# Kernel tuning notes

Hardware: AMD Instinct MI355X
Metric: run time of the kernel (lower is better)

## Reference

```python
import jax, jax.numpy as jnp
import numpy as np

N_NODES = 100000
IN_F = 128
H_F = 128
LOOKBACK = 3
N_EDGES = 640000


def setup_inputs() -> dict:
    key = jax.random.key(0)
    ks = jax.random.split(key, 16)
    s = lambda k, shp: jax.random.normal(k, shp, dtype=jnp.float32) * 0.05
    inp = {
        "feat": jax.random.normal(ks[0], (N_NODES, IN_F), dtype=jnp.float32),
        "edges": jax.random.randint(ks[1], (LOOKBACK, 2, N_EDGES), 0, N_NODES, dtype=jnp.int32),
        # conv1 (SAGEConv pool, in->h) params
        "Wp1": s(ks[2], (IN_F, IN_F)), "bp1": jnp.zeros((IN_F,), jnp.float32),
        "Ws1": s(ks[3], (H_F, IN_F)), "Wn1": s(ks[4], (H_F, IN_F)), "b1": jnp.zeros((H_F,), jnp.float32),
        # BatchNorm1d affine params (training-mode batch stats)
        "gamma": jnp.ones((H_F,), jnp.float32), "beta": jnp.zeros((H_F,), jnp.float32),
        # conv2 (SAGEConv pool, h->h) params
        "Wp2": s(ks[5], (H_F, H_F)), "bp2": jnp.zeros((H_F,), jnp.float32),
        "Ws2": s(ks[6], (H_F, H_F)), "Wn2": s(ks[7], (H_F, H_F)), "b2": jnp.zeros((H_F,), jnp.float32),
    }
    return inp


def _sage_pool_conv(h, src, dst, Wp, bp, Ws, Wn, b):
    # pool aggregator: m = relu(fc_pool(h)); neigh = max over in-edges
    m = jax.nn.relu(h @ Wp.T + bp)                      # [N, d]
    agg = jax.ops.segment_max(m[src], dst, num_segments=N_NODES)  # [N, d]
    agg = jnp.where(jnp.isfinite(agg), agg, 0.0)        # nodes with no in-edges -> 0
    return h @ Ws.T + agg @ Wn.T + b


def _batchnorm(x, gamma, beta, eps=1e-5):
    mu = jnp.mean(x, axis=0)
    var = jnp.var(x, axis=0)
    return (x - mu) * jax.lax.rsqrt(var + eps) * gamma + beta


def reference(feat, edges, Wp1, bp1, Ws1, Wn1, b1, gamma, beta, Wp2, bp2, Ws2, Wn2, b2):
    def per_graph(e):
        src, dst = e[0], e[1]
        h = _sage_pool_conv(feat, src, dst, Wp1, bp1, Ws1, Wn1, b1)
        h = _batchnorm(h, gamma, beta)
        h = jax.nn.relu(h)
        h = _sage_pool_conv(h, src, dst, Wp2, bp2, Ws2, Wn2, b2)
        return h

    return jax.vmap(per_graph)(edges)  # [lookback, N, H_F]
```

## Files before the change

### kernel.cpp

```cpp
#include <hip/hip_runtime.h>
#include <hip/hip_bf16.h>

#define NNODES 100000
#define FD 128
#define NEDGES 640000
#define NB 391
#define NT64 1563
#define GX_TWOA 85
#define GX_ONEW 170
#define GX_HEAD 255
#define OFFS_U32 100032

typedef __bf16 bf16x8 __attribute__((ext_vector_type(8)));
typedef __bf16 bf16x4 __attribute__((ext_vector_type(4)));
typedef float f32x4 __attribute__((ext_vector_type(4)));
typedef unsigned short u16x8 __attribute__((ext_vector_type(8)));

__device__ __forceinline__ bf16x8 cvt8(float4 a, float4 b) {
  bf16x8 r;
  r[0] = (__bf16)a.x; r[1] = (__bf16)a.y; r[2] = (__bf16)a.z; r[3] = (__bf16)a.w;
  r[4] = (__bf16)b.x; r[5] = (__bf16)b.y; r[6] = (__bf16)b.z; r[7] = (__bf16)b.w;
  return r;
}

__device__ __forceinline__ void gl16(const void* g, void* l) {
  __builtin_amdgcn_global_load_lds(
      (const __attribute__((address_space(1))) unsigned int*)g,
      (__attribute__((address_space(3))) unsigned int*)l, 16, 0, 0);
}

__device__ __forceinline__ void stage_w32(const __bf16* Wp, char* l, int wid, int lane) {
#pragma unroll
  for (int i = 0; i < 4; ++i) {
    const int off = (wid * 4 + i) * 1024;
    gl16((const char*)Wp + off + lane * 16, l + off);
  }
}

__device__ __forceinline__ void stage_abf(const __bf16* A, long row0, int M,
                                          char* l, int wid, int lane) {
  long row = row0 + lane;
  if (row > M - 1) row = M - 1;
  const char* base = (const char*)(A + row * FD);
#pragma unroll
  for (int i = 0; i < 2; ++i) {
    const int s = wid * 2 + i;
    gl16(base + s * 16, l + s * 1024);
  }
}

__device__ __forceinline__ void stage_a32(const float* A, long row0, int M,
                                          char* l, int wid, int lane) {
  long row = row0 + lane;
  if (row > M - 1) row = M - 1;
  const char* base = (const char*)(A + row * FD);
#pragma unroll
  for (int i = 0; i < 4; ++i) {
    const int s = wid * 4 + i;
    gl16(base + s * 16, l + s * 1024);
  }
}

__global__ __launch_bounds__(256) void packw6_k(
    const float* __restrict__ W0, const float* __restrict__ W1,
    const float* __restrict__ W2, const float* __restrict__ W3,
    const float* __restrict__ W4, const float* __restrict__ W5,
    __bf16* __restrict__ out) {
  const int gidx = blockIdx.x * 256 + threadIdx.x;
  const int wi = gidx >> 11;
  const int f = gidx & 2047;
  const float* W = wi == 0 ? W0 : wi == 1 ? W1 : wi == 2 ? W2
                 : wi == 3 ? W3 : wi == 4 ? W4 : W5;
  const int c = f >> 8, kk = (f >> 6) & 3, lane = f & 63;
  const int lr = lane & 15, lg = lane >> 4;
  const float* p = W + (c * 16 + lr) * FD + kk * 32 + lg * 8;
  *(bf16x8*)(out + (long)gidx * 8) = cvt8(*(const float4*)p, *(const float4*)(p + 4));
}

template <int AM>
__device__ __forceinline__ void lds_arow(const char* l, int rl, int lg,
                                         const float* __restrict__ scsh,
                                         bf16x8 (&af)[4]) {
#pragma unroll
  for (int kk = 0; kk < 4; ++kk) {
    if constexpr (AM == 0) {
      const int s = kk * 8 + lg * 2;
      const float4 x = *(const float4*)(l + s * 1024 + rl * 16);
      const float4 y = *(const float4*)(l + (s + 1) * 1024 + rl * 16);
      af[kk] = cvt8(x, y);
    } else {
      const bf16x8 r = *(const bf16x8*)(l + (kk * 4 + lg) * 1024 + rl * 16);
      if constexpr (AM == 3) {
        const int k = lg * 8 + kk * 32;
        const float4 scx = *(const float4*)(scsh + k);
        const float4 scy = *(const float4*)(scsh + k + 4);
        const float4 shx = *(const float4*)(scsh + 128 + k);
        const float4 shy = *(const float4*)(scsh + 128 + k + 4);
        bf16x8 o;
        o[0] = (__bf16)fmaxf((float)r[0] * scx.x + shx.x, 0.f);
        o[1] = (__bf16)fmaxf((float)r[1] * scx.y + shx.y, 0.f);
        o[2] = (__bf16)fmaxf((float)r[2] * scx.z + shx.z, 0.f);
        o[3] = (__bf16)fmaxf((float)r[3] * scx.w + shx.w, 0.f);
        o[4] = (__bf16)fmaxf((float)r[4] * scy.x + shy.x, 0.f);
        o[5] = (__bf16)fmaxf((float)r[5] * scy.y + shy.y, 0.f);
        o[6] = (__bf16)fmaxf((float)r[6] * scy.z + shy.z, 0.f);
        o[7] = (__bf16)fmaxf((float)r[7] * scy.w + shy.w, 0.f);
        af[kk] = o;
      } else {
        af[kk] = r;
      }
    }
  }
}

template <int A0M, int A1M, bool TWOA, bool RELU, bool OUTBF16, bool STATS, bool WRITEB>
__global__ __launch_bounds__(512, 1) void gemm_k(
    const void* __restrict__ A0, long a0s, const void* __restrict__ A1, long a1s,
    const __bf16* __restrict__ W0p, const __bf16* __restrict__ W1p,
    const float* __restrict__ bias, const float* __restrict__ scsh0,
    void* __restrict__ outp, long os, float* __restrict__ pblk,
    __bf16* __restrict__ bcopy, int M) {
  constexpr int WSZ = TWOA ? 65536 : 32768;
  constexpr int ASZ = (A0M == 0) ? 32768 : 16384;
  constexpr int A1SZ = TWOA ? 16384 : 0;
  constexpr int LSZ = WSZ + 2 * (ASZ + A1SZ) + (STATS ? 4096 : 0);
  __shared__ __align__(16) char lds[LSZ];
  char* lW0 = lds;
  char* lW1 = lds + 32768;
  char* lA0a = lds + WSZ;
  char* lA1a = lds + WSZ + ASZ;
  char* lA0b = lds + WSZ + ASZ + A1SZ;
  char* lA1b = lds + WSZ + ASZ + A1SZ + ASZ;
  float* s_red = (float*)(lds + WSZ + 2 * (ASZ + A1SZ));

  const int g = blockIdx.y;
  const int tid = threadIdx.x;
  const int wid = tid >> 6;
  const int lane = tid & 63;
  const int rw = wid & 3;
  const int cw = wid >> 2;
  const int lr = lane & 15;
  const int lg = lane >> 4;
  const int S = gridDim.x;

  const void* A0g = (const char*)A0 + (long)g * a0s;
  const void* A1g = (const char*)A1 + (TWOA ? (long)g * a1s : 0);
  void* outg = (char*)outp + (long)g * os;
  const float* scshg = (A0M == 3 || A1M == 3) ? scsh0 + (long)g * 256 : nullptr;

  float ps[4][4], pss[4][4];
  if constexpr (STATS) {
#pragma unroll
    for (int ci = 0; ci < 4; ++ci)
#pragma unroll
      for (int j = 0; j < 4; ++j) { ps[ci][j] = 0.f; pss[ci][j] = 0.f; }
  }

  auto stageA = [&](long t, char* la0, char* la1) {
    if constexpr (A0M == 0) stage_a32((const float*)A0g, t * 64, M, la0, wid, lane);
    else stage_abf((const __bf16*)A0g, t * 64, M, la0, wid, lane);
    if constexpr (TWOA) stage_abf((const __bf16*)A1g, t * 64, M, la1, wid, lane);
  };

  auto body = [&](long t, long tn, char* la0, char* la1, char* na0, char* na1) {
    if (tn < NT64) stageA(tn, na0, na1);
    const int rl = rw * 16 + lr;
    const long row = t * 64 + rl;
    const bool ok = row < M;

    bf16x8 a0f[4];
    lds_arow<A0M>(la0, rl, lg, scshg, a0f);
    bf16x8 a1f[4];
    if constexpr (TWOA) lds_arow<A1M>(la1, rl, lg, scshg, a1f);

    if constexpr (WRITEB) {
      if (cw == 0 && ok) {
#pragma unroll
        for (int kk = 0; kk < 4; ++kk)
          *(bf16x8*)(bcopy + row * FD + lg * 8 + kk * 32) = a0f[kk];
      }
    }

    f32x4 acc[4];
#pragma unroll
    for (int ci = 0; ci < 4; ++ci) acc[ci] = (f32x4){0.f, 0.f, 0.f, 0.f};

#pragma unroll
    for (int ci = 0; ci < 4; ++ci) {
      bf16x8 bw[4];
#pragma unroll
      for (int kk = 0; kk < 4; ++kk)
        bw[kk] = *(const bf16x8*)(lW0 + ((cw * 4 + ci) * 4 + kk) * 1024 + lane * 16);
#pragma unroll
      for (int kk = 0; kk < 4; ++kk)
        acc[ci] = __builtin_amdgcn_mfma_f32_16x16x32_bf16(bw[kk], a0f[kk], acc[ci], 0, 0, 0);
    }
    if constexpr (TWOA) {
#pragma unroll
      for (int ci = 0; ci < 4; ++ci) {
        bf16x8 bw[4];
#pragma unroll
        for (int kk = 0; kk < 4; ++kk)
          bw[kk] = *(const bf16x8*)(lW1 + ((cw * 4 + ci) * 4 + kk) * 1024 + lane * 16);
#pragma unroll
        for (int kk = 0; kk < 4; ++kk)
          acc[ci] = __builtin_amdgcn_mfma_f32_16x16x32_bf16(bw[kk], a1f[kk], acc[ci], 0, 0, 0);
      }
    }

#pragma unroll
    for (int ci = 0; ci < 4; ++ci) {
      const int cb = cw * 64 + ci * 16 + lg * 4;
      f32x4 v = acc[ci];
      if (bias) {
        const float4 bv = *(const float4*)(bias + cb);
        v[0] += bv.x; v[1] += bv.y; v[2] += bv.z; v[3] += bv.w;
      }
      if constexpr (STATS) {
        if (ok) {
#pragma unroll
          for (int j = 0; j < 4; ++j) { ps[ci][j] += v[j]; pss[ci][j] += v[j] * v[j]; }
        }
      }
      if constexpr (RELU) {
#pragma unroll
        for (int j = 0; j < 4; ++j) v[j] = fmaxf(v[j], 0.f);
      }
      if (ok) {
        if constexpr (OUTBF16) {
          bf16x4 o;
          o[0] = (__bf16)v[0]; o[1] = (__bf16)v[1];
          o[2] = (__bf16)v[2]; o[3] = (__bf16)v[3];
          *(bf16x4*)((__bf16*)outg + row * FD + cb) = o;
        } else {
          *(f32x4*)((float*)outg + row * FD + cb) = v;
        }
      }
    }
    __syncthreads();
  };

  stage_w32(W0p, lW0, wid, lane);
  if constexpr (TWOA) stage_w32(W1p, lW1, wid, lane);
  long t = blockIdx.x;
  stageA(t, lA0a, lA1a);
  __syncthreads();

  for (;;) {
    long tn = t + S;
    body(t, tn, lA0a, lA1a, lA0b, lA1b);
    t = tn;
    if (t >= NT64) break;
    tn = t + S;
    body(t, tn, lA0b, lA1b, lA0a, lA1a);
    t = tn;
    if (t >= NT64) break;
  }

  if constexpr (STATS) {
#pragma unroll
    for (int ci = 0; ci < 4; ++ci)
#pragma unroll
      for (int j = 0; j < 4; ++j) {
        float s = ps[ci][j], q = pss[ci][j];
        s += __shfl_xor(s, 1); s += __shfl_xor(s, 2);
        s += __shfl_xor(s, 4); s += __shfl_xor(s, 8);
        q += __shfl_xor(q, 1); q += __shfl_xor(q, 2);
        q += __shfl_xor(q, 4); q += __shfl_xor(q, 8);
        if (lr == 0) {
          s_red[(0 * 8 + wid) * 64 + ci * 16 + lg * 4 + j] = s;
          s_red[(1 * 8 + wid) * 64 + ci * 16 + lg * 4 + j] = q;
        }
      }
    __syncthreads();
    if (tid < 256) {
      const int which = tid >> 7, col = tid & 127;
      const int cwi = col >> 6, cl = col & 63;
      float a = 0.f;
#pragma unroll
      for (int r = 0; r < 4; ++r) a += s_red[(which * 8 + cwi * 4 + r) * 64 + cl];
      pblk[((long)g * gridDim.x + blockIdx.x) * 256 + tid] = a;
    }
  }
}

__global__ __launch_bounds__(256) void bn_final2_k(const float* __restrict__ pblk,
                                                   const float* __restrict__ gamma,
                                                   const float* __restrict__ beta,
                                                   float* __restrict__ scsh3) {
  __shared__ float s_ss[128];
  const int g = blockIdx.y;
  const int tid = threadIdx.x;
  const float* p = pblk + (long)g * GX_TWOA * 256;
  float s = 0.f;
  for (int r = 0; r < GX_TWOA; ++r) s += p[r * 256 + tid];
  if (tid >= 128) s_ss[tid - 128] = s;
  __syncthreads();
  if (tid < 128) {
    const float mu = s / (float)NNODES;
    const float var = s_ss[tid] / (float)NNODES - mu * mu;
    const float sc = rsqrtf(var + 1e-5f) * gamma[tid];
    scsh3[g * 256 + tid] = sc;
    scsh3[g * 256 + 128 + tid] = beta[tid] - mu * sc;
  }
}


__global__ __launch_bounds__(256) void hist_rank3_k(const int* __restrict__ edges,
                                                    unsigned* __restrict__ deg3,
                                                    unsigned short* __restrict__ rank3) {
  const int g = blockIdx.y;
  const int e = blockIdx.x * 256 + threadIdx.x;
  if (e < NEDGES) {
    const int d = edges[(long)g * 2 * NEDGES + NEDGES + e];
    const unsigned r = atomicAdd(&deg3[(long)g * NNODES + d], 1u);
    rank3[(long)g * NEDGES + e] = (unsigned short)r;
  }
}

__global__ __launch_bounds__(256) void blocksum3_k(const unsigned* __restrict__ deg3,
                                                   unsigned* __restrict__ bsum3) {
  __shared__ unsigned s[256];
  const int g = blockIdx.y;
  const int i = blockIdx.x * 256 + threadIdx.x;
  s[threadIdx.x] = (i < NNODES) ? deg3[(long)g * NNODES + i] : 0u;
  __syncthreads();
#pragma unroll
  for (int o = 128; o > 0; o >>= 1) {
    if (threadIdx.x < o) s[threadIdx.x] += s[threadIdx.x + o];
    __syncthreads();
  }
  if (threadIdx.x == 0) bsum3[g * NB + blockIdx.x] = s[0];
}

__global__ __launch_bounds__(512) void scanb3_k(const unsigned* __restrict__ bsum3,
                                                unsigned* __restrict__ boffs3,
                                                unsigned* __restrict__ offs3) {
  __shared__ unsigned s[512];
  const int g = blockIdx.y;
  const unsigned v = (threadIdx.x < NB) ? bsum3[g * NB + threadIdx.x] : 0u;
  s[threadIdx.x] = v;
  __syncthreads();
#pragma unroll
  for (int o = 1; o < 512; o <<= 1) {
    unsigned t = (threadIdx.x >= o) ? s[threadIdx.x - o] : 0u;
    __syncthreads();
    s[threadIdx.x] += t;
    __syncthreads();
  }
  if (threadIdx.x < NB) boffs3[g * NB + threadIdx.x] = s[threadIdx.x] - v;
  if (threadIdx.x == 0) offs3[(long)g * OFFS_U32 + NNODES] = NEDGES;
}

__global__ __launch_bounds__(256) void offsets3_k(const unsigned* __restrict__ deg3,
                                                  const unsigned* __restrict__ boffs3,
                                                  unsigned* __restrict__ offs3) {
  __shared__ unsigned s[256];
  const int g = blockIdx.y;
  const int i = blockIdx.x * 256 + threadIdx.x;
  const unsigned v = (i < NNODES) ? deg3[(long)g * NNODES + i] : 0u;
  s[threadIdx.x] = v;
  __syncthreads();
#pragma unroll
  for (int o = 1; o < 256; o <<= 1) {
    unsigned t = (threadIdx.x >= o) ? s[threadIdx.x - o] : 0u;
    __syncthreads();
    s[threadIdx.x] += t;
    __syncthreads();
  }
  const unsigned excl = s[threadIdx.x] - v + boffs3[g * NB + blockIdx.x];
  if (i < NNODES) offs3[(long)g * OFFS_U32 + i] = excl;
}

__global__ __launch_bounds__(256) void scat3_k(const int* __restrict__ edges,
                                               const unsigned* __restrict__ offs3,
                                               const unsigned short* __restrict__ rank3,
                                               int* __restrict__ ssrc3) {
  const int g = blockIdx.y;
  const int e = blockIdx.x * 256 + threadIdx.x;
  if (e < NEDGES) {
    const int s = edges[(long)g * 2 * NEDGES + e];
    const int d = edges[(long)g * 2 * NEDGES + NEDGES + e];
    const unsigned p = offs3[(long)g * OFFS_U32 + d] + rank3[(long)g * NEDGES + e];
    ssrc3[(long)g * NEDGES + p] = s;
  }
}

__global__ __launch_bounds__(256) void agg_k(const unsigned short* __restrict__ m,
                                             long ms, const int* __restrict__ ssrc3,
                                             const unsigned* __restrict__ offs3,
                                             unsigned short* __restrict__ agg3) {
  const int g = blockIdx.y;
  const unsigned short* mg = m + (long)g * ms;
  const int* ssrc = ssrc3 + (long)g * NEDGES;
  const unsigned* offs = offs3 + (long)g * OFFS_U32;
  unsigned short* agg = agg3 + (long)g * NNODES * FD;

  const int gid = blockIdx.x * 256 + threadIdx.x;
  const int node = gid >> 4;
  if (node >= NNODES) return;
  const int fl = (gid & 15) * 8;
  const unsigned beg = offs[node], end = offs[node + 1];
  u16x8 acc = {0, 0, 0, 0, 0, 0, 0, 0};
  unsigned i = beg;
  for (; i + 2 <= end; i += 2) {
    const int s0 = ssrc[i];
    const int s1 = ssrc[i + 1];
    const u16x8 v0 = *(const u16x8*)(mg + (long)s0 * FD + fl);
    const u16x8 v1 = *(const u16x8*)(mg + (long)s1 * FD + fl);
#pragma unroll
    for (int j = 0; j < 8; ++j) {
      const unsigned short mx = v0[j] > v1[j] ? v0[j] : v1[j];
      acc[j] = mx > acc[j] ? mx : acc[j];
    }
  }
  if (i < end) {
    const u16x8 v = *(const u16x8*)(mg + (long)ssrc[i] * FD + fl);
#pragma unroll
    for (int j = 0; j < 8; ++j) acc[j] = v[j] > acc[j] ? v[j] : acc[j];
  }
  *(u16x8*)(agg + (long)node * FD + fl) = acc;
}

__global__ __launch_bounds__(256) void zero_k(float4* __restrict__ p, long n4) {
  const long i = (long)blockIdx.x * 256 + threadIdx.x;
  if (i < n4) p[i] = (float4){0.f, 0.f, 0.f, 0.f};
}

extern "C" void kernel_launch(void* const* d_in, const int* in_sizes, int n_in,
                              void* d_out, int out_size, void* d_ws, size_t ws_size,
                              hipStream_t stream) {
  const float* feat = (const float*)d_in[0];
  const int* edges = (const int*)d_in[1];
  const float* Wp1 = (const float*)d_in[2];
  const float* bp1 = (const float*)d_in[3];
  const float* Ws1 = (const float*)d_in[4];
  const float* Wn1 = (const float*)d_in[5];
  const float* b1 = (const float*)d_in[6];
  const float* gamma = (const float*)d_in[7];
  const float* beta = (const float*)d_in[8];
  const float* Wp2 = (const float*)d_in[9];
  const float* bp2 = (const float*)d_in[10];
  const float* Ws2 = (const float*)d_in[11];
  const float* Wn2 = (const float*)d_in[12];
  const float* b2 = (const float*)d_in[13];

  const long SZ_BF = 25600000;
  const long SZ_F32 = 51200000;

  char* w = (char*)d_ws;
  __bf16* m1 = (__bf16*)w;
  __bf16* featb = (__bf16*)(w + 25600000);
  __bf16* h1b3 = (__bf16*)(w + 51200000);
  __bf16* aggb3 = (__bf16*)(w + 128000000);
  __bf16* m2_3 = (__bf16*)(w + 204800000);
  float* pblk3 = (float*)(w + 204800000);
  __bf16* wpk = (__bf16*)(w + 281600000);
  float* scsh3 = (float*)(w + 281796608);
  unsigned* deg3 = (unsigned*)(w + 281799680);
  unsigned* offs3 = (unsigned*)(w + 282999680);
  unsigned* bsum3 = (unsigned*)(w + 284200064);
  unsigned* boffs3 = (unsigned*)(w + 284204928);
  unsigned short* rank3 = (unsigned short*)(w + 284209792);
  int* ssrc3 = (int*)(w + 288049792);

  __bf16* Wp1p = wpk;
  __bf16* Ws1p = wpk + 16384;
  __bf16* Wn1p = wpk + 2 * 16384;
  __bf16* Wp2p = wpk + 3 * 16384;
  __bf16* Ws2p = wpk + 4 * 16384;
  __bf16* Wn2p = wpk + 5 * 16384;

  const dim3 blk(256);
  const dim3 blk512(512);
  const int edgeGrid = (NEDGES + 255) / 256;
  const int aggGrid = (NNODES * 16 + 255) / 256;
  const int degZeroGrid = (3 * NNODES / 4 + 255) / 256;

  packw6_k<<<48, blk, 0, stream>>>(Wp1, Ws1, Wn1, Wp2, Ws2, Wn2, wpk);

  zero_k<<<degZeroGrid, blk, 0, stream>>>((float4*)deg3, 3L * NNODES / 4);
  hist_rank3_k<<<dim3(edgeGrid, 3), blk, 0, stream>>>(edges, deg3, rank3);
  blocksum3_k<<<dim3(NB, 3), blk, 0, stream>>>(deg3, bsum3);
  scanb3_k<<<dim3(1, 3), dim3(512), 0, stream>>>(bsum3, boffs3, offs3);
  offsets3_k<<<dim3(NB, 3), blk, 0, stream>>>(deg3, boffs3, offs3);
  scat3_k<<<dim3(edgeGrid, 3), blk, 0, stream>>>(edges, offs3, rank3, ssrc3);

  gemm_k<0, 0, false, true, true, false, true><<<dim3(GX_HEAD, 1), blk512, 0, stream>>>(
      feat, 0, nullptr, 0, Wp1p, nullptr, bp1, nullptr, m1, 0, nullptr, featb, NNODES);

  agg_k<<<dim3(aggGrid, 3), blk, 0, stream>>>((const unsigned short*)m1, 0L,
                                              ssrc3, offs3, (unsigned short*)aggb3);
  gemm_k<1, 1, true, false, true, true, false><<<dim3(GX_TWOA, 3), blk512, 0, stream>>>(
      aggb3, SZ_BF, featb, 0, Wn1p, Ws1p, b1, nullptr, h1b3, SZ_BF, pblk3, nullptr, NNODES);
  bn_final2_k<<<dim3(1, 3), blk, 0, stream>>>(pblk3, gamma, beta, scsh3);

  gemm_k<3, 0, false, true, true, false, false><<<dim3(GX_ONEW, 3), blk512, 0, stream>>>(
      h1b3, SZ_BF, nullptr, 0, Wp2p, nullptr, bp2, scsh3, m2_3, SZ_BF, nullptr, nullptr, NNODES);
  agg_k<<<dim3(aggGrid, 3), blk, 0, stream>>>((const unsigned short*)m2_3,
                                              (long)NNODES * FD, ssrc3, offs3,
                                              (unsigned short*)aggb3);
  gemm_k<3, 1, true, false, false, false, false><<<dim3(GX_TWOA, 3), blk512, 0, stream>>>(
      h1b3, SZ_BF, aggb3, SZ_BF, Ws2p, Wn2p, b2, scsh3, d_out, SZ_F32, nullptr, nullptr, NNODES);
}
```

Baseline: 519.0 us.

## Hold GEMM weights in registers, drop LDS weight staging, double occupancy

```diff
diff --git a/kernel.cpp b/kernel.cpp
--- a/kernel.cpp
+++ b/kernel.cpp
@@ -6,9 +6,9 @@
 #define NEDGES 640000
 #define NB 391
 #define NT64 1563
-#define GX_TWOA 85
-#define GX_ONEW 170
-#define GX_HEAD 255
+#define GX_TWOA 170
+#define GX_ONEW 340
+#define GX_HEAD 512
 #define OFFS_U32 100032
 
 typedef __bf16 bf16x8 __attribute__((ext_vector_type(8)));
@@ -27,14 +27,6 @@
   __builtin_amdgcn_global_load_lds(
       (const __attribute__((address_space(1))) unsigned int*)g,
       (__attribute__((address_space(3))) unsigned int*)l, 16, 0, 0);
-}
-
-__device__ __forceinline__ void stage_w32(const __bf16* Wp, char* l, int wid, int lane) {
-#pragma unroll
-  for (int i = 0; i < 4; ++i) {
-    const int off = (wid * 4 + i) * 1024;
-    gl16((const char*)Wp + off + lane * 16, l + off);
-  }
 }
 
 __device__ __forceinline__ void stage_abf(const __bf16* A, long row0, int M,
@@ -114,31 +106,28 @@
 }
 
 template <int A0M, int A1M, bool TWOA, bool RELU, bool OUTBF16, bool STATS, bool WRITEB>
-__global__ __launch_bounds__(512, 1) void gemm_k(
+__global__ __launch_bounds__(512, 2) void gemm_k(
     const void* __restrict__ A0, long a0s, const void* __restrict__ A1, long a1s,
     const __bf16* __restrict__ W0p, const __bf16* __restrict__ W1p,
     const float* __restrict__ bias, const float* __restrict__ scsh0,
     void* __restrict__ outp, long os, float* __restrict__ pblk,
     __bf16* __restrict__ bcopy, int M) {
-  constexpr int WSZ = TWOA ? 65536 : 32768;
   constexpr int ASZ = (A0M == 0) ? 32768 : 16384;
   constexpr int A1SZ = TWOA ? 16384 : 0;
-  constexpr int LSZ = WSZ + 2 * (ASZ + A1SZ) + (STATS ? 4096 : 0);
+  constexpr int LSZ = 2 * (ASZ + A1SZ) + (STATS ? 2048 : 0);
   __shared__ __align__(16) char lds[LSZ];
-  char* lW0 = lds;
-  char* lW1 = lds + 32768;
-  char* lA0a = lds + WSZ;
-  char* lA1a = lds + WSZ + ASZ;
-  char* lA0b = lds + WSZ + ASZ + A1SZ;
-  char* lA1b = lds + WSZ + ASZ + A1SZ + ASZ;
-  float* s_red = (float*)(lds + WSZ + 2 * (ASZ + A1SZ));
+  char* lA0a = lds;
+  char* lA1a = lds + ASZ;
+  char* lA0b = lds + ASZ + A1SZ;
+  char* lA1b = lds + 2 * ASZ + A1SZ;
+  float* s_red = (float*)(lds + 2 * (ASZ + A1SZ));
 
   const int g = blockIdx.y;
   const int tid = threadIdx.x;
   const int wid = tid >> 6;
   const int lane = tid & 63;
-  const int rw = wid & 3;
-  const int cw = wid >> 2;
+  const int rw = wid & 1;
+  const int cw = wid >> 1;
   const int lr = lane & 15;
   const int lg = lane >> 4;
   const int S = gridDim.x;
@@ -148,10 +137,20 @@
   void* outg = (char*)outp + (long)g * os;
   const float* scshg = (A0M == 3 || A1M == 3) ? scsh0 + (long)g * 256 : nullptr;
 
-  float ps[4][4], pss[4][4];
+  bf16x8 bw0[2][4], bw1[2][4];
+#pragma unroll
+  for (int ci = 0; ci < 2; ++ci)
+#pragma unroll
+    for (int kk = 0; kk < 4; ++kk) {
+      const long f = ((long)((cw * 2 + ci) * 4 + kk) * 64 + lane) * 8;
+      bw0[ci][kk] = *(const bf16x8*)(W0p + f);
+      if constexpr (TWOA) bw1[ci][kk] = *(const bf16x8*)(W1p + f);
+    }
+
+  float ps[2][4], pss[2][4];
   if constexpr (STATS) {
 #pragma unroll
-    for (int ci = 0; ci < 4; ++ci)
+    for (int ci = 0; ci < 2; ++ci)
 #pragma unroll
       for (int j = 0; j < 4; ++j) { ps[ci][j] = 0.f; pss[ci][j] = 0.f; }
   }
@@ -164,84 +163,91 @@
 
   auto body = [&](long t, long tn, char* la0, char* la1, char* na0, char* na1) {
     if (tn < NT64) stageA(tn, na0, na1);
-    const int rl = rw * 16 + lr;
-    const long row = t * 64 + rl;
-    const bool ok = row < M;
-
-    bf16x8 a0f[4];
-    lds_arow<A0M>(la0, rl, lg, scshg, a0f);
-    bf16x8 a1f[4];
-    if constexpr (TWOA) lds_arow<A1M>(la1, rl, lg, scshg, a1f);
+
+    bf16x8 a0f[2][4];
+#pragma unroll
+    for (int tt = 0; tt < 2; ++tt)
+      lds_arow<A0M>(la0, rw * 32 + tt * 16 + lr, lg, scshg, a0f[tt]);
+    bf16x8 a1f[2][4];
+    if constexpr (TWOA) {
+#pragma unroll
+      for (int tt = 0; tt < 2; ++tt)
+        lds_arow<A1M>(la1, rw * 32 + tt * 16 + lr, lg, scshg, a1f[tt]);
+    }
 
     if constexpr (WRITEB) {
-      if (cw == 0 && ok) {
-#pragma unroll
-        for (int kk = 0; kk < 4; ++kk)
-          *(bf16x8*)(bcopy + row * FD + lg * 8 + kk * 32) = a0f[kk];
-      }
-    }
-
-    f32x4 acc[4];
-#pragma unroll
-    for (int ci = 0; ci < 4; ++ci) acc[ci] = (f32x4){0.f, 0.f, 0.f, 0.f};
-
-#pragma unroll
-    for (int ci = 0; ci < 4; ++ci) {
-      bf16x8 bw[4];
-#pragma unroll
-      for (int kk = 0; kk < 4; ++kk)
-        bw[kk] = *(const bf16x8*)(lW0 + ((cw * 4 + ci) * 4 + kk) * 1024 + lane * 16);
-#pragma unroll
-      for (int kk = 0; kk < 4; ++kk)
-        acc[ci] = __builtin_amdgcn_mfma_f32_16x16x32_bf16(bw[kk], a0f[kk], acc[ci], 0, 0, 0);
-    }
-    if constexpr (TWOA) {
-#pragma unroll
-      for (int ci = 0; ci < 4; ++ci) {
-        bf16x8 bw[4];
-#pragma unroll
-        for (int kk = 0; kk < 4; ++kk)
-          bw[kk] = *(const bf16x8*)(lW1 + ((cw * 4 + ci) * 4 + kk) * 1024 + lane * 16);
-#pragma unroll
-        for (int kk = 0; kk < 4; ++kk)
-          acc[ci] = __builtin_amdgcn_mfma_f32_16x16x32_bf16(bw[kk], a1f[kk], acc[ci], 0, 0, 0);
-      }
-    }
-
-#pragma unroll
-    for (int ci = 0; ci < 4; ++ci) {
-      const int cb = cw * 64 + ci * 16 + lg * 4;
-      f32x4 v = acc[ci];
-      if (bias) {
-        const float4 bv = *(const float4*)(bias + cb);
-        v[0] += bv.x; v[1] += bv.y; v[2] += bv.z; v[3] += bv.w;
-      }
-      if constexpr (STATS) {
-        if (ok) {
-#pragma unroll
-          for (int j = 0; j < 4; ++j) { ps[ci][j] += v[j]; pss[ci][j] += v[j] * v[j]; }
+      if (cw == 0) {
+#pragma unroll
+        for (int tt = 0; tt < 2; ++tt) {
+          const long row = t * 64 + rw * 32 + tt * 16 + lr;
+          if (row < M)
+#pragma unroll
+            for (int kk = 0; kk < 4; ++kk)
+              *(bf16x8*)(bcopy + row * FD + lg * 8 + kk * 32) = a0f[tt][kk];
         }
       }
-      if constexpr (RELU) {
-#pragma unroll
-        for (int j = 0; j < 4; ++j) v[j] = fmaxf(v[j], 0.f);
-      }
-      if (ok) {
-        if constexpr (OUTBF16) {
-          bf16x4 o;
-          o[0] = (__bf16)v[0]; o[1] = (__bf16)v[1];
-          o[2] = (__bf16)v[2]; o[3] = (__bf16)v[3];
-          *(bf16x4*)((__bf16*)outg + row * FD + cb) = o;
-        } else {
-          *(f32x4*)((float*)outg + row * FD + cb) = v;
+    }
+
+    f32x4 acc[2][2];
+#pragma unroll
+    for (int tt = 0; tt < 2; ++tt)
+#pragma unroll
+      for (int ci = 0; ci < 2; ++ci) acc[tt][ci] = (f32x4){0.f, 0.f, 0.f, 0.f};
+
+#pragma unroll
+    for (int ci = 0; ci < 2; ++ci)
+#pragma unroll
+      for (int tt = 0; tt < 2; ++tt)
+#pragma unroll
+        for (int kk = 0; kk < 4; ++kk)
+          acc[tt][ci] = __builtin_amdgcn_mfma_f32_16x16x32_bf16(bw0[ci][kk], a0f[tt][kk], acc[tt][ci], 0, 0, 0);
+    if constexpr (TWOA) {
+#pragma unroll
+      for (int ci = 0; ci < 2; ++ci)
+#pragma unroll
+        for (int tt = 0; tt < 2; ++tt)
+#pragma unroll
+          for (int kk = 0; kk < 4; ++kk)
+            acc[tt][ci] = __builtin_amdgcn_mfma_f32_16x16x32_bf16(bw1[ci][kk], a1f[tt][kk], acc[tt][ci], 0, 0, 0);
+    }
+
+#pragma unroll
+    for (int tt = 0; tt < 2; ++tt) {
+      const long row = t * 64 + rw * 32 + tt * 16 + lr;
+      const bool ok = row < M;
+#pragma unroll
+      for (int ci = 0; ci < 2; ++ci) {
+        const int cb = cw * 32 + ci * 16 + lg * 4;
+        f32x4 v = acc[tt][ci];
+        if (bias) {
+          const float4 bv = *(const float4*)(bias + cb);
+          v[0] += bv.x; v[1] += bv.y; v[2] += bv.z; v[3] += bv.w;
+        }
+        if constexpr (STATS) {
+          if (ok) {
+#pragma unroll
+            for (int j = 0; j < 4; ++j) { ps[ci][j] += v[j]; pss[ci][j] += v[j] * v[j]; }
+          }
+        }
+        if constexpr (RELU) {
+#pragma unroll
+          for (int j = 0; j < 4; ++j) v[j] = fmaxf(v[j], 0.f);
+        }
+        if (ok) {
+          if constexpr (OUTBF16) {
+            bf16x4 o;
+            o[0] = (__bf16)v[0]; o[1] = (__bf16)v[1];
+            o[2] = (__bf16)v[2]; o[3] = (__bf16)v[3];
+            *(bf16x4*)((__bf16*)outg + row * FD + cb) = o;
+          } else {
+            *(f32x4*)((float*)outg + row * FD + cb) = v;
+          }
         }
       }
     }
     __syncthreads();
   };
 
-  stage_w32(W0p, lW0, wid, lane);
-  if constexpr (TWOA) stage_w32(W1p, lW1, wid, lane);
   long t = blockIdx.x;
   stageA(t, lA0a, lA1a);
   __syncthreads();
@@ -259,7 +265,7 @@
 
   if constexpr (STATS) {
 #pragma unroll
-    for (int ci = 0; ci < 4; ++ci)
+    for (int ci = 0; ci < 2; ++ci)
 #pragma unroll
       for (int j = 0; j < 4; ++j) {
         float s = ps[ci][j], q = pss[ci][j];
@@ -268,17 +274,16 @@
         q += __shfl_xor(q, 1); q += __shfl_xor(q, 2);
         q += __shfl_xor(q, 4); q += __shfl_xor(q, 8);
         if (lr == 0) {
-          s_red[(0 * 8 + wid) * 64 + ci * 16 + lg * 4 + j] = s;
-          s_red[(1 * 8 + wid) * 64 + ci * 16 + lg * 4 + j] = q;
+          s_red[(0 * 8 + wid) * 32 + ci * 16 + lg * 4 + j] = s;
+          s_red[(1 * 8 + wid) * 32 + ci * 16 + lg * 4 + j] = q;
         }
       }
     __syncthreads();
     if (tid < 256) {
       const int which = tid >> 7, col = tid & 127;
-      const int cwi = col >> 6, cl = col & 63;
-      float a = 0.f;
-#pragma unroll
-      for (int r = 0; r < 4; ++r) a += s_red[(which * 8 + cwi * 4 + r) * 64 + cl];
+      const int cwi = col >> 5, cl = col & 31;
+      const float a = s_red[(which * 8 + cwi * 2 + 0) * 32 + cl] +
+                      s_red[(which * 8 + cwi * 2 + 1) * 32 + cl];
       pblk[((long)g * gridDim.x + blockIdx.x) * 256 + tid] = a;
     }
   }
```

Measured after the change: 529.9 us. +2.1%, slower.
